# Optimization experiments

Measured on AMD Instinct MI355X. Metric: run time of the kernel, lower is better.

## Reference

```python
import jax, jax.numpy as jnp
import numpy as np

EPS_DEN = 1e-7
EPS_SQRT = 1e-12  # clamp before sqrt (torch.cdist matmul-mode also clamps at 0)


def setup_inputs() -> dict:
    key = jax.random.key(0)
    k1, k2 = jax.random.split(key)
    L, N, Q, C = 6, 256, 64, 256
    hs_pair = jax.random.normal(k1, (L, N, Q, C), dtype=jnp.float32)
    centers = jax.random.normal(k2, (L, N, 2, C), dtype=jnp.float32)
    return {"hs_pair": hs_pair, "centers": centers}


def reference(hs_pair, centers):
    # hs_pair: [L, N, Q, C], centers: [L, N, 2, C]
    L, N, Q, C = hs_pair.shape
    x2 = jnp.sum(hs_pair * hs_pair, axis=-1)  # [L, N, Q], constant over iters

    def body(carry, _):
        cen, _prev_a = carry
        c2 = jnp.sum(cen * cen, axis=-1)                     # [L, N, 2]
        xc = jnp.einsum('lnqc,lnkc->lnqk', hs_pair, cen)     # [L, N, Q, 2]
        d2 = x2[..., None] + c2[:, :, None, :] - 2.0 * xc
        dist = jnp.sqrt(jnp.maximum(d2, EPS_SQRT))           # euclidean cdist
        a = jax.nn.softmax(-dist, axis=-1)                   # [L, N, Q, 2]
        num = jnp.einsum('lnqk,lnqc->lnkc', a, hs_pair)      # [L, N, 2, C]
        den = jnp.sum(a, axis=2)                             # [L, N, 2]
        new_cen = num / (den[..., None] + EPS_DEN)
        return (new_cen, a), None

    init_a = jnp.zeros((L, N, Q, 2), dtype=hs_pair.dtype)
    # Q sequential EM iterations; final assignment is the one computed from
    # the centers *before* the last update (matches the torch loop order).
    (centers_out, assignment), _ = jax.lax.scan(body, (centers, init_a), None, length=Q)
    return centers_out, assignment
```

## Files before the change

### kernel.cpp

```cpp
#include <hip/hip_runtime.h>

namespace {
constexpr int PB = 6 * 256;
constexpr int Q = 64;
constexpr int C = 256;
constexpr float EPS_DEN = 1e-7f;
constexpr float EPS_SQRT = 1e-12f;
constexpr int GT_FLOATS = Q * Q;
constexpr int AUX_FLOATS = 256;

typedef __attribute__((ext_vector_type(8))) short bf16x8;
typedef __attribute__((ext_vector_type(4))) float f32x4;

template <int CTRL>
__device__ __forceinline__ float ror_add(float v) {
  int r = __builtin_amdgcn_mov_dpp(__float_as_int(v), CTRL, 0xF, 0xF, true);
  return v + __int_as_float(r);
}

__device__ __forceinline__ float wave_total(float v) {
  v = ror_add<0x121>(v);
  v = ror_add<0x122>(v);
  v = ror_add<0x124>(v);
  v = ror_add<0x128>(v);
  {
    int t = __builtin_amdgcn_update_dpp(0, __float_as_int(v), 0x142, 0xA, 0xF,
                                        true);
    v = v + __int_as_float(t);
  }
  {
    int t = __builtin_amdgcn_update_dpp(0, __float_as_int(v), 0x143, 0xC, 0xF,
                                        true);
    v = v + __int_as_float(t);
  }
  return __int_as_float(__builtin_amdgcn_readlane(__float_as_int(v), 63));
}

__device__ __forceinline__ ushort bf16_rne(float x) {
  uint u = __float_as_uint(x);
  return (ushort)((u + 0x7FFFu + ((u >> 16) & 1u)) >> 16);
}
__device__ __forceinline__ float bf16_up(ushort h) {
  return __uint_as_float((uint)h << 16);
}
}

__global__ __launch_bounds__(256, 2) void k1_gram(
    const float* __restrict__ hs, const float* __restrict__ cen,
    float* __restrict__ ws) {
  const int prob = blockIdx.x;
  const int tid = threadIdx.x;
  const int lane = tid & 63, w = tid >> 6;
  const int li = lane & 15, lk = lane >> 4;

  __shared__ __align__(16) ushort Hh[64 * 128];
  __shared__ __align__(16) ushort Hl[64 * 128];
  __shared__ __align__(16) ushort Ch[2 * 256];
  __shared__ __align__(16) ushort Cl[2 * 256];

  const float4* hsg4 = (const float4*)(hs + (size_t)prob * Q * C);
  float* gtp = ws + (size_t)prob * GT_FLOATS;
  float* aux = ws + (size_t)PB * GT_FLOATS + (size_t)prob * AUX_FLOATS;

  f32x4 acc[4] = {{0.f, 0.f, 0.f, 0.f},
                  {0.f, 0.f, 0.f, 0.f},
                  {0.f, 0.f, 0.f, 0.f},
                  {0.f, 0.f, 0.f, 0.f}};
  f32x4 accX = {0.f, 0.f, 0.f, 0.f};
  const int rA = 16 * w + li;
  const int swz = (li & 7) << 4;

#pragma unroll 1
  for (int half = 0; half < 2; ++half) {
#pragma unroll
    for (int i = 0; i < 8; ++i) {
      const int c = i * 256 + tid;
      const int r = c >> 5, col4 = c & 31;
      float4 v = hsg4[r * 64 + half * 32 + col4];
      ushort h0 = bf16_rne(v.x), h1 = bf16_rne(v.y), h2 = bf16_rne(v.z),
             h3 = bf16_rne(v.w);
      ushort l0 = bf16_rne(v.x - bf16_up(h0));
      ushort l1 = bf16_rne(v.y - bf16_up(h1));
      ushort l2 = bf16_rne(v.z - bf16_up(h2));
      ushort l3 = bf16_rne(v.w - bf16_up(h3));
      const int boff = (col4 * 8) ^ ((r & 7) << 4);
      const int idx = r * 128 + (boff >> 1);
      *(ushort4*)&Hh[idx] = make_ushort4(h0, h1, h2, h3);
      *(ushort4*)&Hl[idx] = make_ushort4(l0, l1, l2, l3);
    }
    if (half == 0) {
      if (tid < 128) {
        const float4* cg4 = (const float4*)(cen + (size_t)prob * 2 * C);
        float4 v = cg4[tid];
        ushort h0 = bf16_rne(v.x), h1 = bf16_rne(v.y), h2 = bf16_rne(v.z),
               h3 = bf16_rne(v.w);
        ushort l0 = bf16_rne(v.x - bf16_up(h0));
        ushort l1 = bf16_rne(v.y - bf16_up(h1));
        ushort l2 = bf16_rne(v.z - bf16_up(h2));
        ushort l3 = bf16_rne(v.w - bf16_up(h3));
        const int idx = (tid >> 6) * 256 + (tid & 63) * 4;
        *(ushort4*)&Ch[idx] = make_ushort4(h0, h1, h2, h3);
        *(ushort4*)&Cl[idx] = make_ushort4(l0, l1, l2, l3);
      }
      float c0v = cen[(size_t)prob * 2 * C + tid];
      float c1v = cen[(size_t)prob * 2 * C + C + tid];
      float p0 = wave_total(c0v * c0v);
      float p1 = wave_total(c1v * c1v);
      if (lane == 0) {
        aux[192 + w] = p0;
        aux[196 + w] = p1;
      }
    }
    __syncthreads();

#pragma unroll
    for (int kk2 = 0; kk2 < 4; ++kk2) {
      const int kk = half * 4 + kk2;
      const int byteA = (kk2 * 64 + lk * 16) ^ swz;
      const int offA = byteA >> 1;
      bf16x8 ah = *(const bf16x8*)&Hh[rA * 128 + offA];
      bf16x8 al = *(const bf16x8*)&Hl[rA * 128 + offA];
      bf16x8 cbh = {0, 0, 0, 0, 0, 0, 0, 0};
      bf16x8 cbl = {0, 0, 0, 0, 0, 0, 0, 0};
      if (li < 2) {
        const int cidx = li * 256 + kk * 32 + lk * 8;
        cbh = *(const bf16x8*)&Ch[cidx];
        cbl = *(const bf16x8*)&Cl[cidx];
      }
      accX = __builtin_amdgcn_mfma_f32_16x16x32_bf16(ah, cbh, accX, 0, 0, 0);
      accX = __builtin_amdgcn_mfma_f32_16x16x32_bf16(ah, cbl, accX, 0, 0, 0);
      accX = __builtin_amdgcn_mfma_f32_16x16x32_bf16(al, cbh, accX, 0, 0, 0);
#pragma unroll
      for (int tj = 0; tj < 4; ++tj) {
        if (tj < w) continue;
        const int rB = 16 * tj + li;
        bf16x8 bh = *(const bf16x8*)&Hh[rB * 128 + offA];
        bf16x8 bl = *(const bf16x8*)&Hl[rB * 128 + offA];
        acc[tj] =
            __builtin_amdgcn_mfma_f32_16x16x32_bf16(ah, bh, acc[tj], 0, 0, 0);
        acc[tj] =
            __builtin_amdgcn_mfma_f32_16x16x32_bf16(ah, bl, acc[tj], 0, 0, 0);
        acc[tj] =
            __builtin_amdgcn_mfma_f32_16x16x32_bf16(al, bh, acc[tj], 0, 0, 0);
      }
    }
    __syncthreads();
  }

#pragma unroll
  for (int tj = 0; tj < 4; ++tj) {
    if (tj < w) continue;
#pragma unroll
    for (int r = 0; r < 4; ++r) {
      const float v = acc[tj][r];
      const int row = 16 * w + lk * 4 + r;
      const int col = 16 * tj + li;
      gtp[(col >> 2) * 256 + row * 4 + (col & 3)] = v;
      if (tj > w) gtp[(row >> 2) * 256 + col * 4 + (row & 3)] = v;
      if (row == col) aux[128 + row] = v;
    }
  }
  if (li < 2) {
#pragma unroll
    for (int r = 0; r < 4; ++r) {
      const int q = 16 * w + lk * 4 + r;
      aux[q * 2 + li] = accX[r];
    }
  }
}

__global__ __launch_bounds__(64, 2) void k2_iter(const float* __restrict__ hs,
                                                 const float* __restrict__ ws,
                                                 float* __restrict__ out) {
  const int prob = blockIdx.x;
  const int lane = threadIdx.x;
  const int li = lane & 15, lk = lane >> 4;

  __shared__ __align__(16) ushort Ah[2][64];
  __shared__ __align__(16) ushort Al[2][64];
  __shared__ __align__(16) float m_s[2][64];
  __shared__ __align__(16) float a_s[2 * Q];

  const float4* gt4 = (const float4*)(ws + (size_t)prob * GT_FLOATS);
  const float* aux = ws + (size_t)PB * GT_FLOATS + (size_t)prob * AUX_FLOATS;

  bf16x8 Gh[4][2], Gl[4][2];
#pragma unroll
  for (int t = 0; t < 4; ++t) {
#pragma unroll
    for (int kk = 0; kk < 2; ++kk) {
      const int cj = 8 * kk + 2 * lk;
      float4 ga = gt4[cj * 64 + 16 * t + li];
      float4 gb = gt4[(cj + 1) * 64 + 16 * t + li];
      float g[8] = {ga.x, ga.y, ga.z, ga.w, gb.x, gb.y, gb.z, gb.w};
      bf16x8 hh, ll;
#pragma unroll
      for (int j = 0; j < 8; ++j) {
        ushort h = bf16_rne(g[j]);
        hh[j] = (short)h;
        ll[j] = (short)bf16_rne(g[j] - bf16_up(h));
      }
      Gh[t][kk] = hh;
      Gl[t][kk] = ll;
    }
  }

  const float x2 = aux[128 + lane];
  float xc0 = aux[lane * 2 + 0];
  float xc1 = aux[lane * 2 + 1];
  float c20 = aux[192] + aux[193] + aux[194] + aux[195];
  float c21 = aux[196] + aux[197] + aux[198] + aux[199];

  float a0 = 0.f, a1 = 0.f;
  const int cl = li & 1;

#pragma unroll 1
  for (int t = 0; t < Q; ++t) {
    float d0 = fmaxf(x2 + c20 - 2.f * xc0, EPS_SQRT);
    float d1 = fmaxf(x2 + c21 - 2.f * xc1, EPS_SQRT);
    float t0 = __builtin_amdgcn_sqrtf(d0), t1 = __builtin_amdgcn_sqrtf(d1);
    float mn = fminf(t0, t1);
    float e0 = __expf(mn - t0), e1 = __expf(mn - t1);
    float inv = __builtin_amdgcn_rcpf(e0 + e1);
    a0 = e0 * inv;
    a1 = e1 * inv;
    if (t == Q - 1) break;

    {
      ushort h0 = bf16_rne(a0);
      ushort l0 = bf16_rne(a0 - bf16_up(h0));
      ushort h1 = bf16_rne(a1);
      ushort l1 = bf16_rne(a1 - bf16_up(h1));
      Ah[0][lane] = h0;
      Al[0][lane] = l0;
      Ah[1][lane] = h1;
      Al[1][lane] = l1;
    }
    float den0 = wave_total(a0);
    float den1 = wave_total(a1);
    __syncthreads();

    bf16x8 bh[2], bl[2];
#pragma unroll
    for (int kk = 0; kk < 2; ++kk) {
      bh[kk] = *(const bf16x8*)&Ah[cl][kk * 32 + lk * 8];
      bl[kk] = *(const bf16x8*)&Al[cl][kk * 32 + lk * 8];
    }
    f32x4 acc[4] = {{0.f, 0.f, 0.f, 0.f},
                    {0.f, 0.f, 0.f, 0.f},
                    {0.f, 0.f, 0.f, 0.f},
                    {0.f, 0.f, 0.f, 0.f}};
#pragma unroll
    for (int tt = 0; tt < 4; ++tt) {
#pragma unroll
      for (int kk = 0; kk < 2; ++kk) {
        acc[tt] = __builtin_amdgcn_mfma_f32_16x16x32_bf16(Gh[tt][kk], bh[kk],
                                                          acc[tt], 0, 0, 0);
        acc[tt] = __builtin_amdgcn_mfma_f32_16x16x32_bf16(Gh[tt][kk], bl[kk],
                                                          acc[tt], 0, 0, 0);
        acc[tt] = __builtin_amdgcn_mfma_f32_16x16x32_bf16(Gl[tt][kk], bh[kk],
                                                          acc[tt], 0, 0, 0);
      }
    }
    if (li < 2) {
#pragma unroll
      for (int tt = 0; tt < 4; ++tt)
        *(float4*)&m_s[li][16 * tt + lk * 4] =
            make_float4(acc[tt][0], acc[tt][1], acc[tt][2], acc[tt][3]);
    }
    __syncthreads();

    float m0 = m_s[0][lane];
    float m1 = m_s[1][lane];
    float s0 = wave_total(a0 * m0);
    float s1 = wave_total(a1 * m1);

    float i0 = __builtin_amdgcn_rcpf(den0 + EPS_DEN);
    float i1 = __builtin_amdgcn_rcpf(den1 + EPS_DEN);
    xc0 = m0 * i0;
    xc1 = m1 * i1;
    c20 = s0 * i0 * i0;
    c21 = s1 * i1 * i1;
  }

  *(float2*)&a_s[lane * 2] = make_float2(a0, a1);
  float den0 = wave_total(a0);
  float den1 = wave_total(a1);
  __syncthreads();
  float i0 = __builtin_amdgcn_rcpf(den0 + EPS_DEN);
  float i1 = __builtin_amdgcn_rcpf(den1 + EPS_DEN);

  const float4* hb4 = (const float4*)(hs + (size_t)prob * Q * C);
  const float2* a2 = (const float2*)a_s;
  float4 n0 = make_float4(0.f, 0.f, 0.f, 0.f);
  float4 n1 = make_float4(0.f, 0.f, 0.f, 0.f);
#pragma unroll 8
  for (int q2 = 0; q2 < Q; ++q2) {
    float4 h = hb4[q2 * 64 + lane];
    float2 aq = a2[q2];
    n0.x = fmaf(aq.x, h.x, n0.x);
    n0.y = fmaf(aq.x, h.y, n0.y);
    n0.z = fmaf(aq.x, h.z, n0.z);
    n0.w = fmaf(aq.x, h.w, n0.w);
    n1.x = fmaf(aq.y, h.x, n1.x);
    n1.y = fmaf(aq.y, h.y, n1.y);
    n1.z = fmaf(aq.y, h.z, n1.z);
    n1.w = fmaf(aq.y, h.w, n1.w);
  }
  float4* outc4 = (float4*)(out + (size_t)prob * 2 * C);
  outc4[lane] = make_float4(n0.x * i0, n0.y * i0, n0.z * i0, n0.w * i0);
  outc4[64 + lane] = make_float4(n1.x * i1, n1.y * i1, n1.z * i1, n1.w * i1);

  float* outa = out + (size_t)PB * 2 * C + (size_t)prob * Q * 2;
  *(float2*)&outa[lane * 2] = make_float2(a0, a1);
}

extern "C" void kernel_launch(void* const* d_in, const int* in_sizes, int n_in,
                              void* d_out, int out_size, void* d_ws,
                              size_t ws_size, hipStream_t stream) {
  const float* hs = (const float*)d_in[0];
  const float* cen = (const float*)d_in[1];
  float* out = (float*)d_out;
  float* ws = (float*)d_ws;
  hipLaunchKernelGGL(k1_gram, dim3(PB), dim3(256), 0, stream, hs, cen, ws);
  hipLaunchKernelGGL(k2_iter, dim3(PB), dim3(64), 0, stream, hs, ws, out);
}
```

Baseline: 92.58 us.

## Process two problems per wave in iteration kernel to interleave dependency chains

The iteration kernel now handles two independent EM problems per 64-thread block, interleaving their softmax, MFMA, reduction and barrier phases so each problem's latency-bound serial chain can overlap with the other's. The grid is halved and launch bounds drop to one block per SIMD hint because register use roughly doubles for the cached Gram fragments. It trades occupancy and block count (768 blocks) for instruction-level parallelism within a wave.

```diff
diff --git a/kernel.cpp b/kernel.cpp
--- a/kernel.cpp
+++ b/kernel.cpp
@@ -169,150 +169,200 @@
   }
 }
 
-__global__ __launch_bounds__(64, 2) void k2_iter(const float* __restrict__ hs,
+__global__ __launch_bounds__(64, 1) void k2_iter(const float* __restrict__ hs,
                                                  const float* __restrict__ ws,
                                                  float* __restrict__ out) {
-  const int prob = blockIdx.x;
+  const int pb = blockIdx.x * 2;
   const int lane = threadIdx.x;
   const int li = lane & 15, lk = lane >> 4;
 
-  __shared__ __align__(16) ushort Ah[2][64];
-  __shared__ __align__(16) ushort Al[2][64];
-  __shared__ __align__(16) float m_s[2][64];
-  __shared__ __align__(16) float a_s[2 * Q];
-
-  const float4* gt4 = (const float4*)(ws + (size_t)prob * GT_FLOATS);
-  const float* aux = ws + (size_t)PB * GT_FLOATS + (size_t)prob * AUX_FLOATS;
-
-  bf16x8 Gh[4][2], Gl[4][2];
-#pragma unroll
-  for (int t = 0; t < 4; ++t) {
-#pragma unroll
-    for (int kk = 0; kk < 2; ++kk) {
-      const int cj = 8 * kk + 2 * lk;
-      float4 ga = gt4[cj * 64 + 16 * t + li];
-      float4 gb = gt4[(cj + 1) * 64 + 16 * t + li];
-      float g[8] = {ga.x, ga.y, ga.z, ga.w, gb.x, gb.y, gb.z, gb.w};
-      bf16x8 hh, ll;
-#pragma unroll
-      for (int j = 0; j < 8; ++j) {
-        ushort h = bf16_rne(g[j]);
-        hh[j] = (short)h;
-        ll[j] = (short)bf16_rne(g[j] - bf16_up(h));
-      }
-      Gh[t][kk] = hh;
-      Gl[t][kk] = ll;
-    }
-  }
-
-  const float x2 = aux[128 + lane];
-  float xc0 = aux[lane * 2 + 0];
-  float xc1 = aux[lane * 2 + 1];
-  float c20 = aux[192] + aux[193] + aux[194] + aux[195];
-  float c21 = aux[196] + aux[197] + aux[198] + aux[199];
-
-  float a0 = 0.f, a1 = 0.f;
+  __shared__ __align__(16) ushort Ah[2][2][64];
+  __shared__ __align__(16) ushort Al[2][2][64];
+  __shared__ __align__(16) float m_s[2][2][64];
+  __shared__ __align__(16) float a_s[2][2 * Q];
+
+  bf16x8 Gh[2][4][2], Gl[2][4][2];
+#pragma unroll
+  for (int P = 0; P < 2; ++P) {
+    const float4* gt4 = (const float4*)(ws + (size_t)(pb + P) * GT_FLOATS);
+#pragma unroll
+    for (int t = 0; t < 4; ++t) {
+#pragma unroll
+      for (int kk = 0; kk < 2; ++kk) {
+        const int cj = 8 * kk + 2 * lk;
+        float4 ga = gt4[cj * 64 + 16 * t + li];
+        float4 gb = gt4[(cj + 1) * 64 + 16 * t + li];
+        float g[8] = {ga.x, ga.y, ga.z, ga.w, gb.x, gb.y, gb.z, gb.w};
+        bf16x8 hh, ll;
+#pragma unroll
+        for (int j = 0; j < 8; ++j) {
+          ushort h = bf16_rne(g[j]);
+          hh[j] = (short)h;
+          ll[j] = (short)bf16_rne(g[j] - bf16_up(h));
+        }
+        Gh[P][t][kk] = hh;
+        Gl[P][t][kk] = ll;
+      }
+    }
+  }
+
+  float x2[2], xc0[2], xc1[2], c20[2], c21[2], a0[2], a1[2];
+#pragma unroll
+  for (int P = 0; P < 2; ++P) {
+    const float* aux =
+        ws + (size_t)PB * GT_FLOATS + (size_t)(pb + P) * AUX_FLOATS;
+    x2[P] = aux[128 + lane];
+    xc0[P] = aux[lane * 2 + 0];
+    xc1[P] = aux[lane * 2 + 1];
+    c20[P] = aux[192] + aux[193] + aux[194] + aux[195];
+    c21[P] = aux[196] + aux[197] + aux[198] + aux[199];
+    a0[P] = 0.f;
+    a1[P] = 0.f;
+  }
+
   const int cl = li & 1;
 
 #pragma unroll 1
   for (int t = 0; t < Q; ++t) {
-    float d0 = fmaxf(x2 + c20 - 2.f * xc0, EPS_SQRT);
-    float d1 = fmaxf(x2 + c21 - 2.f * xc1, EPS_SQRT);
-    float t0 = __builtin_amdgcn_sqrtf(d0), t1 = __builtin_amdgcn_sqrtf(d1);
-    float mn = fminf(t0, t1);
-    float e0 = __expf(mn - t0), e1 = __expf(mn - t1);
-    float inv = __builtin_amdgcn_rcpf(e0 + e1);
-    a0 = e0 * inv;
-    a1 = e1 * inv;
+#pragma unroll
+    for (int P = 0; P < 2; ++P) {
+      float d0 = fmaxf(x2[P] + c20[P] - 2.f * xc0[P], EPS_SQRT);
+      float d1 = fmaxf(x2[P] + c21[P] - 2.f * xc1[P], EPS_SQRT);
+      float t0 = __builtin_amdgcn_sqrtf(d0), t1 = __builtin_amdgcn_sqrtf(d1);
+      float mn = fminf(t0, t1);
+      float e0 = __expf(mn - t0), e1 = __expf(mn - t1);
+      float inv = __builtin_amdgcn_rcpf(e0 + e1);
+      a0[P] = e0 * inv;
+      a1[P] = e1 * inv;
+    }
     if (t == Q - 1) break;
 
-    {
-      ushort h0 = bf16_rne(a0);
-      ushort l0 = bf16_rne(a0 - bf16_up(h0));
-      ushort h1 = bf16_rne(a1);
-      ushort l1 = bf16_rne(a1 - bf16_up(h1));
-      Ah[0][lane] = h0;
-      Al[0][lane] = l0;
-      Ah[1][lane] = h1;
-      Al[1][lane] = l1;
-    }
-    float den0 = wave_total(a0);
-    float den1 = wave_total(a1);
+#pragma unroll
+    for (int P = 0; P < 2; ++P) {
+      ushort h0 = bf16_rne(a0[P]);
+      ushort l0 = bf16_rne(a0[P] - bf16_up(h0));
+      ushort h1 = bf16_rne(a1[P]);
+      ushort l1 = bf16_rne(a1[P] - bf16_up(h1));
+      Ah[P][0][lane] = h0;
+      Al[P][0][lane] = l0;
+      Ah[P][1][lane] = h1;
+      Al[P][1][lane] = l1;
+    }
+    float den0[2], den1[2];
+#pragma unroll
+    for (int P = 0; P < 2; ++P) {
+      den0[P] = wave_total(a0[P]);
+      den1[P] = wave_total(a1[P]);
+    }
     __syncthreads();
 
-    bf16x8 bh[2], bl[2];
-#pragma unroll
-    for (int kk = 0; kk < 2; ++kk) {
-      bh[kk] = *(const bf16x8*)&Ah[cl][kk * 32 + lk * 8];
-      bl[kk] = *(const bf16x8*)&Al[cl][kk * 32 + lk * 8];
-    }
-    f32x4 acc[4] = {{0.f, 0.f, 0.f, 0.f},
-                    {0.f, 0.f, 0.f, 0.f},
-                    {0.f, 0.f, 0.f, 0.f},
-                    {0.f, 0.f, 0.f, 0.f}};
+    bf16x8 bh[2][2], bl[2][2];
+#pragma unroll
+    for (int P = 0; P < 2; ++P) {
+#pragma unroll
+      for (int kk = 0; kk < 2; ++kk) {
+        bh[P][kk] = *(const bf16x8*)&Ah[P][cl][kk * 32 + lk * 8];
+        bl[P][kk] = *(const bf16x8*)&Al[P][cl][kk * 32 + lk * 8];
+      }
+    }
+    f32x4 acc[2][4];
+#pragma unroll
+    for (int P = 0; P < 2; ++P)
+#pragma unroll
+      for (int tt = 0; tt < 4; ++tt) acc[P][tt] = {0.f, 0.f, 0.f, 0.f};
 #pragma unroll
     for (int tt = 0; tt < 4; ++tt) {
 #pragma unroll
-      for (int kk = 0; kk < 2; ++kk) {
-        acc[tt] = __builtin_amdgcn_mfma_f32_16x16x32_bf16(Gh[tt][kk], bh[kk],
-                                                          acc[tt], 0, 0, 0);
-        acc[tt] = __builtin_amdgcn_mfma_f32_16x16x32_bf16(Gh[tt][kk], bl[kk],
-                                                          acc[tt], 0, 0, 0);
-        acc[tt] = __builtin_amdgcn_mfma_f32_16x16x32_bf16(Gl[tt][kk], bh[kk],
-                                                          acc[tt], 0, 0, 0);
+      for (int P = 0; P < 2; ++P) {
+#pragma unroll
+        for (int kk = 0; kk < 2; ++kk) {
+          acc[P][tt] = __builtin_amdgcn_mfma_f32_16x16x32_bf16(
+              Gh[P][tt][kk], bh[P][kk], acc[P][tt], 0, 0, 0);
+          acc[P][tt] = __builtin_amdgcn_mfma_f32_16x16x32_bf16(
+              Gh[P][tt][kk], bl[P][kk], acc[P][tt], 0, 0, 0);
+          acc[P][tt] = __builtin_amdgcn_mfma_f32_16x16x32_bf16(
+              Gl[P][tt][kk], bh[P][kk], acc[P][tt], 0, 0, 0);
+        }
       }
     }
     if (li < 2) {
 #pragma unroll
-      for (int tt = 0; tt < 4; ++tt)
-        *(float4*)&m_s[li][16 * tt + lk * 4] =
-            make_float4(acc[tt][0], acc[tt][1], acc[tt][2], acc[tt][3]);
+      for (int P = 0; P < 2; ++P)
+#pragma unroll
+        for (int tt = 0; tt < 4; ++tt)
+          *(float4*)&m_s[P][li][16 * tt + lk * 4] = make_float4(
+              acc[P][tt][0], acc[P][tt][1], acc[P][tt][2], acc[P][tt][3]);
     }
     __syncthreads();
 
-    float m0 = m_s[0][lane];
-    float m1 = m_s[1][lane];
-    float s0 = wave_total(a0 * m0);
-    float s1 = wave_total(a1 * m1);
-
-    float i0 = __builtin_amdgcn_rcpf(den0 + EPS_DEN);
-    float i1 = __builtin_amdgcn_rcpf(den1 + EPS_DEN);
-    xc0 = m0 * i0;
-    xc1 = m1 * i1;
-    c20 = s0 * i0 * i0;
-    c21 = s1 * i1 * i1;
-  }
-
-  *(float2*)&a_s[lane * 2] = make_float2(a0, a1);
-  float den0 = wave_total(a0);
-  float den1 = wave_total(a1);
+    float m0[2], m1[2], s0[2], s1[2];
+#pragma unroll
+    for (int P = 0; P < 2; ++P) {
+      m0[P] = m_s[P][0][lane];
+      m1[P] = m_s[P][1][lane];
+    }
+#pragma unroll
+    for (int P = 0; P < 2; ++P) {
+      s0[P] = wave_total(a0[P] * m0[P]);
+      s1[P] = wave_total(a1[P] * m1[P]);
+    }
+#pragma unroll
+    for (int P = 0; P < 2; ++P) {
+      float i0 = __builtin_amdgcn_rcpf(den0[P] + EPS_DEN);
+      float i1 = __builtin_amdgcn_rcpf(den1[P] + EPS_DEN);
+      xc0[P] = m0[P] * i0;
+      xc1[P] = m1[P] * i1;
+      c20[P] = s0[P] * i0 * i0;
+      c21[P] = s1[P] * i1 * i1;
+    }
+  }
+
+#pragma unroll
+  for (int P = 0; P < 2; ++P)
+    *(float2*)&a_s[P][lane * 2] = make_float2(a0[P], a1[P]);
+  float den0[2], den1[2];
+#pragma unroll
+  for (int P = 0; P < 2; ++P) {
+    den0[P] = wave_total(a0[P]);
+    den1[P] = wave_total(a1[P]);
+  }
   __syncthreads();
-  float i0 = __builtin_amdgcn_rcpf(den0 + EPS_DEN);
-  float i1 = __builtin_amdgcn_rcpf(den1 + EPS_DEN);
-
-  const float4* hb4 = (const float4*)(hs + (size_t)prob * Q * C);
-  const float2* a2 = (const float2*)a_s;
-  float4 n0 = make_float4(0.f, 0.f, 0.f, 0.f);
-  float4 n1 = make_float4(0.f, 0.f, 0.f, 0.f);
-#pragma unroll 8
+
+  float4 n0[2], n1[2];
+#pragma unroll
+  for (int P = 0; P < 2; ++P) {
+    n0[P] = make_float4(0.f, 0.f, 0.f, 0.f);
+    n1[P] = make_float4(0.f, 0.f, 0.f, 0.f);
+  }
+#pragma unroll 4
   for (int q2 = 0; q2 < Q; ++q2) {
-    float4 h = hb4[q2 * 64 + lane];
-    float2 aq = a2[q2];
-    n0.x = fmaf(aq.x, h.x, n0.x);
-    n0.y = fmaf(aq.x, h.y, n0.y);
-    n0.z = fmaf(aq.x, h.z, n0.z);
-    n0.w = fmaf(aq.x, h.w, n0.w);
-    n1.x = fmaf(aq.y, h.x, n1.x);
-    n1.y = fmaf(aq.y, h.y, n1.y);
-    n1.z = fmaf(aq.y, h.z, n1.z);
-    n1.w = fmaf(aq.y, h.w, n1.w);
-  }
-  float4* outc4 = (float4*)(out + (size_t)prob * 2 * C);
-  outc4[lane] = make_float4(n0.x * i0, n0.y * i0, n0.z * i0, n0.w * i0);
-  outc4[64 + lane] = make_float4(n1.x * i1, n1.y * i1, n1.z * i1, n1.w * i1);
-
-  float* outa = out + (size_t)PB * 2 * C + (size_t)prob * Q * 2;
-  *(float2*)&outa[lane * 2] = make_float2(a0, a1);
+#pragma unroll
+    for (int P = 0; P < 2; ++P) {
+      const float4* hb4 = (const float4*)(hs + (size_t)(pb + P) * Q * C);
+      float4 h = hb4[q2 * 64 + lane];
+      float2 aq = *(const float2*)&a_s[P][q2 * 2];
+      n0[P].x = fmaf(aq.x, h.x, n0[P].x);
+      n0[P].y = fmaf(aq.x, h.y, n0[P].y);
+      n0[P].z = fmaf(aq.x, h.z, n0[P].z);
+      n0[P].w = fmaf(aq.x, h.w, n0[P].w);
+      n1[P].x = fmaf(aq.y, h.x, n1[P].x);
+      n1[P].y = fmaf(aq.y, h.y, n1[P].y);
+      n1[P].z = fmaf(aq.y, h.z, n1[P].z);
+      n1[P].w = fmaf(aq.y, h.w, n1[P].w);
+    }
+  }
+#pragma unroll
+  for (int P = 0; P < 2; ++P) {
+    float i0 = __builtin_amdgcn_rcpf(den0[P] + EPS_DEN);
+    float i1 = __builtin_amdgcn_rcpf(den1[P] + EPS_DEN);
+    float4* outc4 = (float4*)(out + (size_t)(pb + P) * 2 * C);
+    outc4[lane] =
+        make_float4(n0[P].x * i0, n0[P].y * i0, n0[P].z * i0, n0[P].w * i0);
+    outc4[64 + lane] =
+        make_float4(n1[P].x * i1, n1[P].y * i1, n1[P].z * i1, n1[P].w * i1);
+    float* outa = out + (size_t)PB * 2 * C + (size_t)(pb + P) * Q * 2;
+    *(float2*)&outa[lane * 2] = make_float2(a0[P], a1[P]);
+  }
 }
 
 extern "C" void kernel_launch(void* const* d_in, const int* in_sizes, int n_in,
@@ -323,5 +373,5 @@
   float* out = (float*)d_out;
   float* ws = (float*)d_ws;
   hipLaunchKernelGGL(k1_gram, dim3(PB), dim3(256), 0, stream, hs, cen, ws);
-  hipLaunchKernelGGL(k2_iter, dim3(PB), dim3(64), 0, stream, hs, ws, out);
-}
+  hipLaunchKernelGGL(k2_iter, dim3(PB / 2), dim3(64), 0, stream, hs, ws, out);
+}
```

After: 113.5 us. +22.6%, slower.
